# Kernel tuning notes

Measured on AMD Instinct MI355X. Metric: run time of the kernel, lower is better.

## Reference

```python
import jax, jax.numpy as jnp
import numpy as np

B, S, D = 4, 2048, 1024
H = 16
HS = D // H  # 64


def setup_inputs() -> dict:
    key = jax.random.key(0)
    ks = jax.random.split(key, 6)
    scale = 1.0 / np.sqrt(D)
    x = jax.random.normal(ks[0], (B, S, D), dtype=jnp.float32)
    # per-head projection weights, stacked: [H, D, HS]
    Wq = jax.random.normal(ks[1], (H, D, HS), dtype=jnp.float32) * scale
    Wk = jax.random.normal(ks[2], (H, D, HS), dtype=jnp.float32) * scale
    Wv = jax.random.normal(ks[3], (H, D, HS), dtype=jnp.float32) * scale
    Wo = jax.random.normal(ks[4], (D, D), dtype=jnp.float32) * scale
    bo = jax.random.normal(ks[5], (D,), dtype=jnp.float32) * 0.01
    return {"x": x, "Wq": Wq, "Wk": Wk, "Wv": Wv, "Wo": Wo, "bo": bo}


def reference(x, Wq, Wk, Wv, Wo, bo):
    # Per-head dense projections (no bias): [B,S,D] x [H,D,HS] -> [B,H,S,HS]
    q = jnp.einsum('bsd,hde->bhse', x, Wq)
    k = jnp.einsum('bsd,hde->bhse', x, Wk)
    v = jnp.einsum('bsd,hde->bhse', x, Wv)
    # scaled dot-product scores: [B,H,S,S]
    scores = jnp.einsum('bhse,bhte->bhst', q, k) / jnp.sqrt(jnp.asarray(HS, dtype=x.dtype))
    # causal mask (lower triangular kept)
    causal = jnp.tril(jnp.ones((S, S), dtype=bool))
    scores = jnp.where(causal, scores, -jnp.inf)
    attn = jax.nn.softmax(scores, axis=-1)
    # dropout is identity at inference (rate handled as 0)
    out = jnp.einsum('bhst,bhte->bhse', attn, v)  # [B,H,S,HS]
    # concat heads: [B,S,H*HS] = [B,S,D]
    out = jnp.transpose(out, (0, 2, 1, 3)).reshape(B, S, D)
    return out @ Wo + bo
```

## Files before the change

kernel.cpp:

```cpp
#include <hip/hip_runtime.h>
#include <hip/hip_bf16.h>
#include <stdint.h>

#define NB 4
#define NS 2048
#define ND 1024
#define NH 16
#define NHS 64
#define NEG_BIG (-1e30f)
#define Q_SCALE 0.18033688011112042f

typedef __bf16 bf16x8 __attribute__((ext_vector_type(8)));
typedef float floatx4 __attribute__((ext_vector_type(4)));
typedef short s16x4 __attribute__((ext_vector_type(4)));

#if defined(__has_builtin)
#if __has_builtin(__builtin_amdgcn_mfma_f32_16x16x16bf16_1k)
#define HAVE_MFMA1K 1
#endif
#endif
#ifndef HAVE_MFMA1K
#define HAVE_MFMA1K 0
#endif

static constexpr size_t WSLAB = (size_t)NH * ND * NHS;
static constexpr size_t QSLAB = (size_t)NB * NH * NS * NHS;
static constexpr size_t XSLAB = (size_t)NB * NS * ND;

__device__ __forceinline__ uint16_t f2b(float f) {
    union { __hip_bfloat16 h; uint16_t u; } cv;
    cv.h = __float2bfloat16(f);
    return cv.u;
}

__device__ __forceinline__ void gll16(const void* g, void* l) {
  __builtin_amdgcn_global_load_lds(
      (__attribute__((address_space(1))) void*)(uintptr_t)g,
      (__attribute__((address_space(3))) void*)(uintptr_t)l,
      16, 0, 0);
}

__global__ __launch_bounds__(256) void k_prep(
    const float* __restrict__ x, const float* __restrict__ Wq,
    const float* __restrict__ Wk, const float* __restrict__ Wv,
    const float* __restrict__ Wo, uint16_t* __restrict__ xb,
    uint16_t* __restrict__ wt) {
  __shared__ __align__(16) uint16_t T[64][72];
  int bid = blockIdx.x;
  int tid = threadIdx.x;
  if (bid < 4096) {
    size_t i0 = ((size_t)bid * 256 + tid) * 8;
    float4 f0 = *(const float4*)&x[i0];
    float4 f1 = *(const float4*)&x[i0 + 4];
    __align__(16) uint16_t tmp[8];
    tmp[0] = f2b(f0.x); tmp[1] = f2b(f0.y); tmp[2] = f2b(f0.z); tmp[3] = f2b(f0.w);
    tmp[4] = f2b(f1.x); tmp[5] = f2b(f1.y); tmp[6] = f2b(f1.z); tmp[7] = f2b(f1.w);
    *(uint4*)&xb[i0] = *(uint4*)tmp;
    return;
  }
  bid -= 4096;
  const float* src; uint16_t* dst;
  int srcStride, dstStride, r0, c0;
  if (bid < 768) {
    int mat = bid >> 8;
    int rem = bid & 255;
    int h = rem >> 4, dt = rem & 15;
    const float* W = (mat == 0) ? Wq : (mat == 1) ? Wk : Wv;
    src = W + (size_t)h * (ND * NHS);
    dst = wt + (size_t)mat * WSLAB + (size_t)h * (NHS * ND);
    srcStride = NHS; dstStride = ND;
    r0 = dt * 64; c0 = 0;
  } else {
    int rem = bid - 768;
    int dt = rem >> 4, et = rem & 15;
    src = Wo; dst = wt + 3 * WSLAB;
    srcStride = ND; dstStride = ND;
    r0 = dt * 64; c0 = et * 64;
  }
  for (int u = tid; u < 1024; u += 256) {
    int row = u >> 4, cq = u & 15;
    float4 f = *(const float4*)&src[(size_t)(r0 + row) * srcStride + c0 + cq * 4];
    uint16_t* p = &T[row][cq * 4];
    p[0] = f2b(f.x); p[1] = f2b(f.y); p[2] = f2b(f.z); p[3] = f2b(f.w);
  }
  __syncthreads();
  for (int u = tid; u < 512; u += 256) {
    int c = u >> 3, cg = u & 7;
    __align__(16) uint16_t tmp[8];
    for (int j = 0; j < 8; j++) tmp[j] = T[cg * 8 + j][c];
    *(uint4*)&dst[(size_t)(c0 + c) * dstStride + r0 + cg * 8] = *(uint4*)tmp;
  }
}

__global__ __launch_bounds__(512, 4) void k_qkv(
    const uint16_t* __restrict__ xb, const uint16_t* __restrict__ wt,
    uint16_t* __restrict__ qk, uint16_t* __restrict__ vt) {
  __shared__ __align__(16) uint16_t L[32768];

  int bid = blockIdx.x;
  int xcd = bid & 7, idx = bid >> 3;
  int mtile = xcd * 8 + (idx & 7);
  int ntile = idx >> 3;
  int m0 = mtile * 128;
  int n0 = ntile * 128;

  int tid = threadIdx.x;
  int wave = tid >> 6, lane = tid & 63, quad = lane >> 4, l16 = lane & 15;
  int wr = wave >> 2, wc = wave & 3;

  int swc = ((tid & 3) ^ ((tid >> 4) & 3)) * 8;
  const uint16_t* pA = xb + (size_t)(m0 + (tid >> 2)) * ND + swc;
  const uint16_t* pB = wt + (size_t)(n0 + (tid >> 2)) * ND + swc;
  const int stOff = wave * 512;

  const int rq = (quad ^ (l16 >> 2)) * 8;
  const int offA = (wr * 64 + l16) * 32 + rq;
  const int offB = (wc * 32 + l16) * 32 + rq;

  floatx4 acc[4][2];
  #pragma unroll
  for (int i = 0; i < 4; i++)
    #pragma unroll
    for (int j = 0; j < 2; j++) acc[i][j] = (floatx4){0.f, 0.f, 0.f, 0.f};

#define STAGE(A_)                                                               \
  do {                                                                          \
    int a_ = (A_);                                                              \
    if (a_ < 32) {                                                              \
      int ko_ = (a_ >> 1) * 64 + (a_ & 1) * 32;                                 \
      gll16(pA + ko_, &L[(a_ & 3) * 4096 + stOff]);                             \
      gll16(pB + ko_, &L[16384 + (a_ & 3) * 4096 + stOff]);                     \
    }                                                                           \
  } while (0)

#define PH_BAR()                         \
  do {                                   \
    asm volatile("" ::: "memory");       \
    __builtin_amdgcn_s_barrier();        \
    asm volatile("" ::: "memory");       \
  } while (0)

  STAGE(0); STAGE(1); STAGE(2);
  asm volatile("s_waitcnt vmcnt(4)" ::: "memory");
  PH_BAR();

#define MFMA8()                                                                           \
  _Pragma("unroll")                                                                       \
  for (int mt_ = 0; mt_ < 4; mt_++)                                                       \
    _Pragma("unroll")                                                                     \
    for (int nt_ = 0; nt_ < 2; nt_++)                                                     \
      acc[mt_][nt_] = __builtin_amdgcn_mfma_f32_16x16x32_bf16(af[mt_], bfr[nt_], acc[mt_][nt_], 0, 0, 0)

  for (int t = 0; t < 16; ++t) {
    {
      int sA = ((2 * t) & 3) * 4096;
      int sB = 16384 + ((2 * t) & 3) * 4096;
      bf16x8 af[4], bfr[2];
      #pragma unroll
      for (int i = 0; i < 4; i++) af[i] = *(const bf16x8*)&L[sA + offA + i * 512];
      #pragma unroll
      for (int i = 0; i < 2; i++) bfr[i] = *(const bf16x8*)&L[sB + offB + i * 512];
      STAGE(2 * t + 3);
      PH_BAR();
      __builtin_amdgcn_s_setprio(1);
      MFMA8();
      __builtin_amdgcn_s_setprio(0);
      if (t < 15) { asm volatile("s_waitcnt vmcnt(4)" ::: "memory"); }
      else        { asm volatile("s_waitcnt vmcnt(0)" ::: "memory"); }
      PH_BAR();
    }
    {
      int sA = ((2 * t + 1) & 3) * 4096;
      int sB = 16384 + ((2 * t + 1) & 3) * 4096;
      bf16x8 af[4], bfr[2];
      #pragma unroll
      for (int i = 0; i < 4; i++) af[i] = *(const bf16x8*)&L[sA + offA + i * 512];
      #pragma unroll
      for (int i = 0; i < 2; i++) bfr[i] = *(const bf16x8*)&L[sB + offB + i * 512];
      STAGE(2 * t + 4);
      PH_BAR();
      __builtin_amdgcn_s_setprio(1);
      MFMA8();
      __builtin_amdgcn_s_setprio(0);
      if (t < 14)       { asm volatile("s_waitcnt vmcnt(4)" ::: "memory"); }
      else if (t == 14) { asm volatile("s_waitcnt vmcnt(2)" ::: "memory"); }
      if (t < 15) PH_BAR();
    }
  }
#undef MFMA8
#undef STAGE
#undef PH_BAR

  int matid = n0 >> 10;
  int b = m0 >> 11;
  if (matid == 2) {
    int hh = ((n0 - 2048) >> 6) + (wc >> 1);
    #pragma unroll
    for (int nt = 0; nt < 2; nt++) {
      int e = (wc & 1) * 32 + nt * 16 + l16;
      uint16_t* vrow = vt + ((size_t)(b * 16 + hh) * 64 + e) * NS;
      #pragma unroll
      for (int mt = 0; mt < 4; mt++) {
        __align__(8) uint16_t t4v[4];
        #pragma unroll
        for (int r = 0; r < 4; r++) t4v[r] = f2b(acc[mt][nt][r]);
        int s = (m0 & 2047) + wr * 64 + mt * 16 + quad * 4;
        *(uint2*)&vrow[s] = *(uint2*)t4v;
      }
    }
  } else {
    float scale = (matid == 0) ? Q_SCALE : 1.0f;
    uint16_t* base = qk + (size_t)matid * QSLAB;
    int hh = ((n0 & 1023) >> 6) + (wc >> 1);
    #pragma unroll
    for (int mt = 0; mt < 4; mt++) {
      int s = (m0 & 2047) + wr * 64 + mt * 16 + quad * 4;
      size_t rbase = ((size_t)(b * 16 + hh) * NS + s) * NHS;
      #pragma unroll
      for (int nt = 0; nt < 2; nt++)
        #pragma unroll
        for (int r = 0; r < 4; r++)
          base[rbase + (size_t)r * NHS + (wc & 1) * 32 + nt * 16 + l16] =
              f2b(acc[mt][nt][r] * scale);
    }
  }
}

#if HAVE_MFMA1K
__global__ __launch_bounds__(256, 4) void k_attn(
    const uint16_t* __restrict__ Q, const uint16_t* __restrict__ K,
    const uint16_t* __restrict__ VT, uint16_t* __restrict__ Y) {
  __shared__ __align__(16) uint16_t Ks[2][4096];
  __shared__ __align__(16) uint16_t Vs[2][4096];
  int bh = blockIdx.y;
  int b = bh >> 4, h = bh & 15;
  int ta = blockIdx.x;
  int tb = 31 - ta;
  const uint16_t* Qp = Q + (size_t)bh * (NS * NHS);
  const uint16_t* Kp = K + (size_t)bh * (NS * NHS);
  const uint16_t* Vp = VT + (size_t)bh * (NS * NHS);
  int tid = threadIdx.x;
  int wv = tid >> 6, lane = tid & 63, quad = lane >> 4, l16 = lane & 15;

  int srow = lane >> 3;
  int swOff = ((lane & 7) ^ srow) * 8;
  int stRow0 = wv * 16 + srow;
  int stRow1 = wv * 16 + 8 + srow;
  const int dst0 = wv * 1024;
  const int dst1 = wv * 1024 + 512;

#define STAGE_KV(KT, BUF)                                                         \
  do {                                                                            \
    int kt_ = (KT);                                                               \
    gll16(Kp + (size_t)(kt_ * 64 + stRow0) * NHS + swOff, &Ks[BUF][dst0]);        \
    gll16(Kp + (size_t)(kt_ * 64 + stRow1) * NHS + swOff, &Ks[BUF][dst1]);        \
    gll16(Vp + (size_t)stRow0 * NS + kt_ * 64 + swOff, &Vs[BUF][dst0]);           \
    gll16(Vp + (size_t)stRow1 * NS + kt_ * 64 + swOff, &Vs[BUF][dst1]);           \
  } while (0)

  int e3 = l16 & 7;
  int kc0 = (quad ^ e3) * 8;
  int kc1 = ((4 | quad) ^ e3) * 8;
  int vql = (quad & 1) * 4;
  int vqh = quad >> 1;
  int vcol[4];
  #pragma unroll
  for (int ct = 0; ct < 4; ct++)
    vcol[ct] = (((ct * 2 + vqh) ^ e3) * 8) + vql;

  int rA = ta * 64 + wv * 16 + l16;
  int rB = tb * 64 + wv * 16 + l16;
  bf16x8 aqA0 = *(const bf16x8*)&Qp[(size_t)rA * NHS + quad * 8];
  bf16x8 aqA1 = *(const bf16x8*)&Qp[(size_t)rA * NHS + 32 + quad * 8];
  bf16x8 aqB0 = *(const bf16x8*)&Qp[(size_t)rB * NHS + quad * 8];
  bf16x8 aqB1 = *(const bf16x8*)&Qp[(size_t)rB * NHS + 32 + quad * 8];

  float lAs = 0.f, lBs = 0.f;
  floatx4 oA[4], oB[4];
  for (int et = 0; et < 4; et++) {
    oA[et] = (floatx4){0.f, 0.f, 0.f, 0.f};
    oB[et] = (floatx4){0.f, 0.f, 0.f, 0.f};
  }

  STAGE_KV(0, 0);
  __syncthreads();

  for (int kt = 0; kt <= tb; kt++) {
    int cur = kt & 1;
    if (kt < tb) STAGE_KV(kt + 1, cur ^ 1);
    const uint16_t* KB = &Ks[cur][0];
    const uint16_t* VB = &Vs[cur][0];
    bool doA = (kt <= ta);

    s16x4 pbA[4], pbB[4];
    #pragma unroll
    for (int ct = 0; ct < 4; ct++) {
      int krow = (ct * 16 + l16) * 64;
      bf16x8 kb0 = *(const bf16x8*)&KB[krow + kc0];
      bf16x8 kb1 = *(const bf16x8*)&KB[krow + kc1];
      int key = kt * 64 + ct * 16 + quad * 4;
      floatx4 c = (floatx4){0.f, 0.f, 0.f, 0.f};
      c = __builtin_amdgcn_mfma_f32_16x16x32_bf16(kb0, aqB0, c, 0, 0, 0);
      c = __builtin_amdgcn_mfma_f32_16x16x32_bf16(kb1, aqB1, c, 0, 0, 0);
      #pragma unroll
      for (int r = 0; r < 4; r++) {
        float s = (kt == tb && key + r > rB) ? NEG_BIG : c[r];
        float p = __builtin_amdgcn_exp2f(s);
        lBs += p;
        pbB[ct][r] = (short)f2b(p);
      }
      if (doA) {
        floatx4 d = (floatx4){0.f, 0.f, 0.f, 0.f};
        d = __builtin_amdgcn_mfma_f32_16x16x32_bf16(kb0, aqA0, d, 0, 0, 0);
        d = __builtin_amdgcn_mfma_f32_16x16x32_bf16(kb1, aqA1, d, 0, 0, 0);
        #pragma unroll
        for (int r = 0; r < 4; r++) {
          float s = (kt == ta && key + r > rA) ? NEG_BIG : d[r];
          float p = __builtin_amdgcn_exp2f(s);
          lAs += p;
          pbA[ct][r] = (short)f2b(p);
        }
      }
    }
    #pragma unroll
    for (int et = 0; et < 4; et++) {
      int vrow = (et * 16 + l16) * 64;
      #pragma unroll
      for (int ct = 0; ct < 4; ct++) {
        s16x4 va = *(const s16x4*)&VB[vrow + vcol[ct]];
        oB[et] = __builtin_amdgcn_mfma_f32_16x16x16bf16_1k(va, pbB[ct], oB[et], 0, 0, 0);
        if (doA)
          oA[et] = __builtin_amdgcn_mfma_f32_16x16x16bf16_1k(va, pbA[ct], oA[et], 0, 0, 0);
      }
    }
    __syncthreads();
  }
#undef STAGE_KV

  lAs += __shfl_xor(lAs, 16, 64); lAs += __shfl_xor(lAs, 32, 64);
  lBs += __shfl_xor(lBs, 16, 64); lBs += __shfl_xor(lBs, 32, 64);
  float invA = 1.f / lAs, invB = 1.f / lBs;
  uint16_t* yb = Y + (size_t)b * NS * ND + (size_t)h * NHS;
  for (int et = 0; et < 4; et++) {
    __align__(8) uint16_t tA[4], tB[4];
    for (int r = 0; r < 4; r++) {
      tA[r] = f2b(oA[et][r] * invA);
      tB[r] = f2b(oB[et][r] * invB);
    }
    *(uint2*)&yb[(size_t)rA * ND + et * 16 + quad * 4] = *(uint2*)tA;
    *(uint2*)&yb[(size_t)rB * ND + et * 16 + quad * 4] = *(uint2*)tB;
  }
}
#else
__global__ __launch_bounds__(256) void k_attn(
    const uint16_t* __restrict__ Q, const uint16_t* __restrict__ K,
    const uint16_t* __restrict__ VT, uint16_t* __restrict__ Y) {
  __shared__ __align__(16) uint16_t Ks[64][72];
  __shared__ __align__(16) uint16_t Vs[64][72];
  __shared__ __align__(16) uint16_t Ps[4][2][16][72];
  int bh = blockIdx.y;
  int b = bh >> 4, h = bh & 15;
  int ta = blockIdx.x;
  int tb = 31 - ta;
  const uint16_t* Qp = Q + (size_t)bh * (NS * NHS);
  const uint16_t* Kp = K + (size_t)bh * (NS * NHS);
  const uint16_t* Vp = VT + (size_t)bh * (NS * NHS);
  int tid = threadIdx.x;
  int wv = tid >> 6, lane = tid & 63, quad = lane >> 4, l16 = lane & 15;

  int rA = ta * 64 + wv * 16 + l16;
  int rB = tb * 64 + wv * 16 + l16;
  bf16x8 aqA0 = *(const bf16x8*)&Qp[(size_t)rA * NHS + quad * 8];
  bf16x8 aqA1 = *(const bf16x8*)&Qp[(size_t)rA * NHS + 32 + quad * 8];
  bf16x8 aqB0 = *(const bf16x8*)&Qp[(size_t)rB * NHS + quad * 8];
  bf16x8 aqB1 = *(const bf16x8*)&Qp[(size_t)rB * NHS + 32 + quad * 8];

  float lA[4] = {0.f, 0.f, 0.f, 0.f}, lB[4] = {0.f, 0.f, 0.f, 0.f};
  floatx4 oA[4], oB[4];
  for (int ct = 0; ct < 4; ct++) {
    oA[ct] = (floatx4){0.f, 0.f, 0.f, 0.f};
    oB[ct] = (floatx4){0.f, 0.f, 0.f, 0.f};
  }
  for (int kt = 0; kt <= tb; kt++) {
    bool doA = (kt <= ta);
    __syncthreads();
    for (int u = tid; u < 512; u += 256) {
      int row = u >> 3, cg = u & 7;
      *(uint4*)&Ks[row][cg * 8] =
          *(const uint4*)&Kp[(size_t)(kt * 64 + row) * NHS + cg * 8];
    }
    for (int u = tid; u < 512; u += 256) {
      int row = u >> 3, cg = u & 7;
      *(uint4*)&Vs[row][cg * 8] =
          *(const uint4*)&Vp[(size_t)row * NS + kt * 64 + cg * 8];
    }
    __syncthreads();
    floatx4 sA[4], sB[4];
    for (int ct = 0; ct < 4; ct++) {
      bf16x8 kb0 = *(const bf16x8*)&Ks[ct * 16 + l16][quad * 8];
      bf16x8 kb1 = *(const bf16x8*)&Ks[ct * 16 + l16][32 + quad * 8];
      floatx4 c = (floatx4){0.f, 0.f, 0.f, 0.f};
      c = __builtin_amdgcn_mfma_f32_16x16x32_bf16(aqB0, kb0, c, 0, 0, 0);
      c = __builtin_amdgcn_mfma_f32_16x16x32_bf16(aqB1, kb1, c, 0, 0, 0);
      sB[ct] = c;
      if (doA) {
        floatx4 d = (floatx4){0.f, 0.f, 0.f, 0.f};
        d = __builtin_amdgcn_mfma_f32_16x16x32_bf16(aqA0, kb0, d, 0, 0, 0);
        d = __builtin_amdgcn_mfma_f32_16x16x32_bf16(aqA1, kb1, d, 0, 0, 0);
        sA[ct] = d;
      }
    }
    if (kt == tb) {
      int qrb = tb * 64 + wv * 16 + quad * 4;
      for (int ct = 0; ct < 4; ct++) {
        int kg = kt * 64 + ct * 16 + l16;
        for (int r = 0; r < 4; r++)
          sB[ct][r] = (kg <= qrb + r) ? sB[ct][r] : NEG_BIG;
      }
    }
    if (doA && kt == ta) {
      int qrb = ta * 64 + wv * 16 + quad * 4;
      for (int ct = 0; ct < 4; ct++) {
        int kg = kt * 64 + ct * 16 + l16;
        for (int r = 0; r < 4; r++)
          sA[ct][r] = (kg <= qrb + r) ? sA[ct][r] : NEG_BIG;
      }
    }
    for (int ct = 0; ct < 4; ct++)
      for (int r = 0; r < 4; r++) {
        float p = __builtin_amdgcn_exp2f(sB[ct][r]);
        lB[r] += p;
        Ps[wv][1][quad * 4 + r][ct * 16 + l16] = f2b(p);
      }
    if (doA)
      for (int ct = 0; ct < 4; ct++)
        for (int r = 0; r < 4; r++) {
          float p = __builtin_amdgcn_exp2f(sA[ct][r]);
          lA[r] += p;
          Ps[wv][0][quad * 4 + r][ct * 16 + l16] = f2b(p);
        }
    bf16x8 apB0 = *(const bf16x8*)&Ps[wv][1][l16][quad * 8];
    bf16x8 apB1 = *(const bf16x8*)&Ps[wv][1][l16][32 + quad * 8];
    bf16x8 apA0, apA1;
    if (doA) {
      apA0 = *(const bf16x8*)&Ps[wv][0][l16][quad * 8];
      apA1 = *(const bf16x8*)&Ps[wv][0][l16][32 + quad * 8];
    }
    for (int ct = 0; ct < 4; ct++) {
      bf16x8 vb0 = *(const bf16x8*)&Vs[ct * 16 + l16][quad * 8];
      bf16x8 vb1 = *(const bf16x8*)&Vs[ct * 16 + l16][32 + quad * 8];
      oB[ct] = __builtin_amdgcn_mfma_f32_16x16x32_bf16(apB0, vb0, oB[ct], 0, 0, 0);
      oB[ct] = __builtin_amdgcn_mfma_f32_16x16x32_bf16(apB1, vb1, oB[ct], 0, 0, 0);
      if (doA) {
        oA[ct] = __builtin_amdgcn_mfma_f32_16x16x32_bf16(apA0, vb0, oA[ct], 0, 0, 0);
        oA[ct] = __builtin_amdgcn_mfma_f32_16x16x32_bf16(apA1, vb1, oA[ct], 0, 0, 0);
      }
    }
  }
  for (int off = 1; off < 16; off <<= 1)
    for (int r = 0; r < 4; r++) {
      lA[r] += __shfl_xor(lA[r], off, 64);
      lB[r] += __shfl_xor(lB[r], off, 64);
    }
  uint16_t* yb = Y + (size_t)b * NS * ND + (size_t)h * NHS;
  for (int ct = 0; ct < 4; ct++)
    for (int r = 0; r < 4; r++) {
      int sA_ = ta * 64 + wv * 16 + quad * 4 + r;
      int sB_ = tb * 64 + wv * 16 + quad * 4 + r;
      yb[(size_t)sA_ * ND + ct * 16 + l16] = f2b(oA[ct][r] / lA[r]);
      yb[(size_t)sB_ * ND + ct * 16 + l16] = f2b(oB[ct][r] / lB[r]);
    }
}
#endif

__global__ __launch_bounds__(512, 4) void k_proj(
    const uint16_t* __restrict__ y, const uint16_t* __restrict__ wot,
    const float* __restrict__ bo, float* __restrict__ out) {
  __shared__ __align__(16) uint16_t L[32768];

  int bid = blockIdx.x;
  int xcd = bid & 7, idx = bid >> 3;
  int mtile = xcd * 8 + (idx & 7);
  int ntile = idx >> 3;
  int m0 = mtile * 128;
  int n0 = ntile * 128;

  int tid = threadIdx.x;
  int wave = tid >> 6, lane = tid & 63, quad = lane >> 4, l16 = lane & 15;
  int wr = wave >> 2, wc = wave & 3;

  int swc = ((tid & 3) ^ ((tid >> 4) & 3)) * 8;
  const uint16_t* pA = y + (size_t)(m0 + (tid >> 2)) * ND + swc;
  const uint16_t* pB = wot + (size_t)(n0 + (tid >> 2)) * ND + swc;
  const int stOff = wave * 512;

  const int rq = (quad ^ (l16 >> 2)) * 8;
  const int offA = (wr * 64 + l16) * 32 + rq;
  const int offB = (wc * 32 + l16) * 32 + rq;

  floatx4 acc[4][2];
  #pragma unroll
  for (int i = 0; i < 4; i++)
    #pragma unroll
    for (int j = 0; j < 2; j++) acc[i][j] = (floatx4){0.f, 0.f, 0.f, 0.f};

#define STAGE(A_)                                                               \
  do {                                                                          \
    int a_ = (A_);                                                              \
    if (a_ < 32) {                                                              \
      int ko_ = (a_ >> 1) * 64 + (a_ & 1) * 32;                                 \
      gll16(pA + ko_, &L[(a_ & 3) * 4096 + stOff]);                             \
      gll16(pB + ko_, &L[16384 + (a_ & 3) * 4096 + stOff]);                     \
    }                                                                           \
  } while (0)

#define PH_BAR()                         \
  do {                                   \
    asm volatile("" ::: "memory");       \
    __builtin_amdgcn_s_barrier();        \
    asm volatile("" ::: "memory");       \
  } while (0)

  STAGE(0); STAGE(1); STAGE(2);
  asm volatile("s_waitcnt vmcnt(4)" ::: "memory");
  PH_BAR();

#define MFMA8()                                                                           \
  _Pragma("unroll")                                                                       \
  for (int mt_ = 0; mt_ < 4; mt_++)                                                       \
    _Pragma("unroll")                                                                     \
    for (int nt_ = 0; nt_ < 2; nt_++)                                                     \
      acc[mt_][nt_] = __builtin_amdgcn_mfma_f32_16x16x32_bf16(af[mt_], bfr[nt_], acc[mt_][nt_], 0, 0, 0)

  for (int t = 0; t < 16; ++t) {
    {
      int sA = ((2 * t) & 3) * 4096;
      int sB = 16384 + ((2 * t) & 3) * 4096;
      bf16x8 af[4], bfr[2];
      #pragma unroll
      for (int i = 0; i < 4; i++) af[i] = *(const bf16x8*)&L[sA + offA + i * 512];
      #pragma unroll
      for (int i = 0; i < 2; i++) bfr[i] = *(const bf16x8*)&L[sB + offB + i * 512];
      STAGE(2 * t + 3);
      PH_BAR();
      __builtin_amdgcn_s_setprio(1);
      MFMA8();
      __builtin_amdgcn_s_setprio(0);
      if (t < 15) { asm volatile("s_waitcnt vmcnt(4)" ::: "memory"); }
      else        { asm volatile("s_waitcnt vmcnt(0)" ::: "memory"); }
      PH_BAR();
    }
    {
      int sA = ((2 * t + 1) & 3) * 4096;
      int sB = 16384 + ((2 * t + 1) & 3) * 4096;
      bf16x8 af[4], bfr[2];
      #pragma unroll
      for (int i = 0; i < 4; i++) af[i] = *(const bf16x8*)&L[sA + offA + i * 512];
      #pragma unroll
      for (int i = 0; i < 2; i++) bfr[i] = *(const bf16x8*)&L[sB + offB + i * 512];
      STAGE(2 * t + 4);
      PH_BAR();
      __builtin_amdgcn_s_setprio(1);
      MFMA8();
      __builtin_amdgcn_s_setprio(0);
      if (t < 14)       { asm volatile("s_waitcnt vmcnt(4)" ::: "memory"); }
      else if (t == 14) { asm volatile("s_waitcnt vmcnt(2)" ::: "memory"); }
      if (t < 15) PH_BAR();
    }
  }
#undef MFMA8
#undef STAGE
#undef PH_BAR

  float bv[2];
  #pragma unroll
  for (int nt = 0; nt < 2; nt++) bv[nt] = bo[n0 + wc * 32 + nt * 16 + l16];
  #pragma unroll
  for (int mt = 0; mt < 4; mt++) {
    int s = m0 + wr * 64 + mt * 16 + quad * 4;
    #pragma unroll
    for (int nt = 0; nt < 2; nt++) {
      int n = n0 + wc * 32 + nt * 16 + l16;
      #pragma unroll
      for (int r = 0; r < 4; r++)
        out[(size_t)(s + r) * ND + n] = acc[mt][nt][r] + bv[nt];
    }
  }
}

extern "C" void kernel_launch(void* const* d_in, const int* in_sizes, int n_in,
                              void* d_out, int out_size, void* d_ws, size_t ws_size,
                              hipStream_t stream) {
  const float* x  = (const float*)d_in[0];
  const float* Wq = (const float*)d_in[1];
  const float* Wk = (const float*)d_in[2];
  const float* Wv = (const float*)d_in[3];
  const float* Wo = (const float*)d_in[4];
  const float* bo = (const float*)d_in[5];
  uint16_t* ws = (uint16_t*)d_ws;

  uint16_t* wt = ws;
  uint16_t* xb = ws + 4 * WSLAB;
  uint16_t* q  = xb + XSLAB;
  uint16_t* k  = q + QSLAB;
  uint16_t* vt = k + QSLAB;
  uint16_t* y  = vt + QSLAB;

  k_prep<<<dim3(5120), dim3(256), 0, stream>>>(x, Wq, Wk, Wv, Wo, xb, wt);
  k_qkv<<<dim3(1536), dim3(512), 0, stream>>>(xb, wt, q, vt);
  k_attn<<<dim3(16, NB * NH), dim3(256), 0, stream>>>(q, k, vt, y);
  k_proj<<<dim3(512), dim3(512), 0, stream>>>(y, wt + 3 * WSLAB, bo, (float*)d_out);
}
```

Measured before the change: 250.6 us.

## Enlarge QKV GEMM tile to 256x128 with triple-buffered 64-wide K stages

The QKV projection GEMM now uses 256-row output tiles instead of 128. Each wave accumulates 8x2 MFMA tiles, and the grid is halved to 768 blocks. Shared memory grows to hold three 64-wide K stages, and the prefetch/wait/barrier schedule is rewritten to issue loads two K-steps ahead with one barrier per half-step. This aims to raise arithmetic intensity per loaded weight tile and cut barriers, at the cost of more registers, lower occupancy (launch bound 2) and fewer blocks for load balance.

After: 253.5 us. About the same (+1.1%).

```diff
diff --git a/kernel.cpp b/kernel.cpp
--- a/kernel.cpp
+++ b/kernel.cpp
@@ -92,16 +92,16 @@
   }
 }
 
-__global__ __launch_bounds__(512, 4) void k_qkv(
+__global__ __launch_bounds__(512, 2) void k_qkv(
     const uint16_t* __restrict__ xb, const uint16_t* __restrict__ wt,
     uint16_t* __restrict__ qk, uint16_t* __restrict__ vt) {
-  __shared__ __align__(16) uint16_t L[32768];
+  __shared__ __align__(16) uint16_t L[73728];
 
   int bid = blockIdx.x;
   int xcd = bid & 7, idx = bid >> 3;
-  int mtile = xcd * 8 + (idx & 7);
-  int ntile = idx >> 3;
-  int m0 = mtile * 128;
+  int mtile = xcd * 4 + (idx & 3);
+  int ntile = idx >> 2;
+  int m0 = mtile * 256;
   int n0 = ntile * 128;
 
   int tid = threadIdx.x;
@@ -111,25 +111,31 @@
   int swc = ((tid & 3) ^ ((tid >> 4) & 3)) * 8;
   const uint16_t* pA = xb + (size_t)(m0 + (tid >> 2)) * ND + swc;
   const uint16_t* pB = wt + (size_t)(n0 + (tid >> 2)) * ND + swc;
-  const int stOff = wave * 512;
+  const int stOff = tid * 8;
 
   const int rq = (quad ^ (l16 >> 2)) * 8;
-  const int offA = (wr * 64 + l16) * 32 + rq;
-  const int offB = (wc * 32 + l16) * 32 + rq;
-
-  floatx4 acc[4][2];
+  const int offA = wr * 4096 + l16 * 32 + rq;
+  const int offB = l16 * 32 + rq;
+
+  floatx4 acc[8][2];
   #pragma unroll
-  for (int i = 0; i < 4; i++)
+  for (int i = 0; i < 8; i++)
     #pragma unroll
     for (int j = 0; j < 2; j++) acc[i][j] = (floatx4){0.f, 0.f, 0.f, 0.f};
 
-#define STAGE(A_)                                                               \
+#define SA(T, KK, P)                                                            \
   do {                                                                          \
-    int a_ = (A_);                                                              \
-    if (a_ < 32) {                                                              \
-      int ko_ = (a_ >> 1) * 64 + (a_ & 1) * 32;                                 \
-      gll16(pA + ko_, &L[(a_ & 3) * 4096 + stOff]);                             \
-      gll16(pB + ko_, &L[16384 + (a_ & 3) * 4096 + stOff]);                     \
+    if ((T) < 16) {                                                             \
+      int kb_ = (T) * 64 + (KK) * 32;                                           \
+      gll16(pA + kb_, &L[((P) * 2 + (KK)) * 8192 + stOff]);                     \
+      gll16(pA + 128 * ND + kb_, &L[((P) * 2 + (KK)) * 8192 + 4096 + stOff]);   \
+    }                                                                           \
+  } while (0)
+#define SB(T, KK, P)                                                            \
+  do {                                                                          \
+    if ((T) < 16) {                                                             \
+      int kb_ = (T) * 64 + (KK) * 32;                                           \
+      gll16(pB + kb_, &L[49152 + ((P) * 2 + (KK)) * 4096 + stOff]);             \
     }                                                                           \
   } while (0)
 
@@ -140,55 +146,60 @@
     asm volatile("" ::: "memory");       \
   } while (0)
 
-  STAGE(0); STAGE(1); STAGE(2);
-  asm volatile("s_waitcnt vmcnt(4)" ::: "memory");
+  SA(0, 0, 0); SB(0, 0, 0);
+  SA(0, 1, 0); SB(0, 1, 0);
+  SA(1, 0, 1); SB(1, 0, 1);
+  SA(1, 1, 1); SB(1, 1, 1);
+  asm volatile("s_waitcnt vmcnt(9)" ::: "memory");
   PH_BAR();
 
-#define MFMA8()                                                                           \
+#define MFMA16()                                                                          \
   _Pragma("unroll")                                                                       \
-  for (int mt_ = 0; mt_ < 4; mt_++)                                                       \
+  for (int mt_ = 0; mt_ < 8; mt_++)                                                       \
     _Pragma("unroll")                                                                     \
     for (int nt_ = 0; nt_ < 2; nt_++)                                                     \
       acc[mt_][nt_] = __builtin_amdgcn_mfma_f32_16x16x32_bf16(af[mt_], bfr[nt_], acc[mt_][nt_], 0, 0, 0)
 
+  int p = 0, p2 = 2;
   for (int t = 0; t < 16; ++t) {
     {
-      int sA = ((2 * t) & 3) * 4096;
-      int sB = 16384 + ((2 * t) & 3) * 4096;
-      bf16x8 af[4], bfr[2];
-      #pragma unroll
-      for (int i = 0; i < 4; i++) af[i] = *(const bf16x8*)&L[sA + offA + i * 512];
-      #pragma unroll
-      for (int i = 0; i < 2; i++) bfr[i] = *(const bf16x8*)&L[sB + offB + i * 512];
-      STAGE(2 * t + 3);
+      int aB = (p * 2 + 0) * 8192;
+      int bB = 49152 + (p * 2 + 0) * 4096 + (wc * 32) * 32;
+      bf16x8 af[8], bfr[2];
+      #pragma unroll
+      for (int i = 0; i < 8; i++) af[i] = *(const bf16x8*)&L[aB + offA + i * 512];
+      #pragma unroll
+      for (int i = 0; i < 2; i++) bfr[i] = *(const bf16x8*)&L[bB + offB + i * 512];
+      SA(t + 2, 0, p2); SB(t + 2, 0, p2);
+      if (t <= 13)      { asm volatile("s_waitcnt vmcnt(9)" ::: "memory"); }
+      else if (t == 14) { asm volatile("s_waitcnt vmcnt(6)" ::: "memory"); }
+      else              { asm volatile("s_waitcnt vmcnt(0)" ::: "memory"); }
       PH_BAR();
       __builtin_amdgcn_s_setprio(1);
-      MFMA8();
+      MFMA16();
       __builtin_amdgcn_s_setprio(0);
-      if (t < 15) { asm volatile("s_waitcnt vmcnt(4)" ::: "memory"); }
-      else        { asm volatile("s_waitcnt vmcnt(0)" ::: "memory"); }
-      PH_BAR();
     }
     {
-      int sA = ((2 * t + 1) & 3) * 4096;
-      int sB = 16384 + ((2 * t + 1) & 3) * 4096;
-      bf16x8 af[4], bfr[2];
-      #pragma unroll
-      for (int i = 0; i < 4; i++) af[i] = *(const bf16x8*)&L[sA + offA + i * 512];
-      #pragma unroll
-      for (int i = 0; i < 2; i++) bfr[i] = *(const bf16x8*)&L[sB + offB + i * 512];
-      STAGE(2 * t + 4);
-      PH_BAR();
+      int aB = (p * 2 + 1) * 8192;
+      int bB = 49152 + (p * 2 + 1) * 4096 + (wc * 32) * 32;
+      bf16x8 af[8], bfr[2];
+      #pragma unroll
+      for (int i = 0; i < 8; i++) af[i] = *(const bf16x8*)&L[aB + offA + i * 512];
+      #pragma unroll
+      for (int i = 0; i < 2; i++) bfr[i] = *(const bf16x8*)&L[bB + offB + i * 512];
+      SA(t + 2, 1, p2); SB(t + 2, 1, p2);
+      if (t <= 13)      { asm volatile("s_waitcnt vmcnt(9)" ::: "memory"); PH_BAR(); }
+      else if (t == 14) { asm volatile("s_waitcnt vmcnt(3)" ::: "memory"); PH_BAR(); }
       __builtin_amdgcn_s_setprio(1);
-      MFMA8();
+      MFMA16();
       __builtin_amdgcn_s_setprio(0);
-      if (t < 14)       { asm volatile("s_waitcnt vmcnt(4)" ::: "memory"); }
-      else if (t == 14) { asm volatile("s_waitcnt vmcnt(2)" ::: "memory"); }
-      if (t < 15) PH_BAR();
-    }
-  }
-#undef MFMA8
-#undef STAGE
+    }
+    p = (p == 2) ? 0 : p + 1;
+    p2 = (p2 == 2) ? 0 : p2 + 1;
+  }
+#undef MFMA16
+#undef SA
+#undef SB
 #undef PH_BAR
 
   int matid = n0 >> 10;
@@ -200,11 +211,11 @@
       int e = (wc & 1) * 32 + nt * 16 + l16;
       uint16_t* vrow = vt + ((size_t)(b * 16 + hh) * 64 + e) * NS;
       #pragma unroll
-      for (int mt = 0; mt < 4; mt++) {
+      for (int mt = 0; mt < 8; mt++) {
         __align__(8) uint16_t t4v[4];
         #pragma unroll
         for (int r = 0; r < 4; r++) t4v[r] = f2b(acc[mt][nt][r]);
-        int s = (m0 & 2047) + wr * 64 + mt * 16 + quad * 4;
+        int s = (m0 & 2047) + wr * 128 + mt * 16 + quad * 4;
         *(uint2*)&vrow[s] = *(uint2*)t4v;
       }
     }
@@ -213,8 +224,8 @@
     uint16_t* base = qk + (size_t)matid * QSLAB;
     int hh = ((n0 & 1023) >> 6) + (wc >> 1);
     #pragma unroll
-    for (int mt = 0; mt < 4; mt++) {
-      int s = (m0 & 2047) + wr * 64 + mt * 16 + quad * 4;
+    for (int mt = 0; mt < 8; mt++) {
+      int s = (m0 & 2047) + wr * 128 + mt * 16 + quad * 4;
       size_t rbase = ((size_t)(b * 16 + hh) * NS + s) * NHS;
       #pragma unroll
       for (int nt = 0; nt < 2; nt++)
@@ -607,7 +618,7 @@
   uint16_t* y  = vt + QSLAB;
 
   k_prep<<<dim3(5120), dim3(256), 0, stream>>>(x, Wq, Wk, Wv, Wo, xb, wt);
-  k_qkv<<<dim3(1536), dim3(512), 0, stream>>>(xb, wt, q, vt);
+  k_qkv<<<dim3(768), dim3(512), 0, stream>>>(xb, wt, q, vt);
   k_attn<<<dim3(16, NB * NH), dim3(256), 0, stream>>>(q, k, vt, y);
   k_proj<<<dim3(512), dim3(512), 0, stream>>>(y, wt + 3 * WSLAB, bo, (float*)d_out);
 }
```
